# Kernel tuning notes

Measured on AMD Instinct MI355X. Metric: run time of the kernel, lower is better.

Reference implementation:

```python
import jax, jax.numpy as jnp
import numpy as np

Z_DIM = 3
H = 128
N_BLOCKS = 4
N = 30000
E = 180000
T = 2


def _mlp2(x, W1, b1, W2, b2):
    return jnp.maximum(x @ W1 + b1, 0.0) @ W2 + b2


def _stats(x, eps=1e-8):
    # batch mean/std as accumulated by the running-stat Normalizer (buffers -> no grad)
    m = x.mean(0)
    v = jnp.maximum((x * x).mean(0) - m * m, 0.0)
    s = jnp.maximum(jnp.sqrt(v), eps)
    return jax.lax.stop_gradient(m), jax.lax.stop_gradient(s)


def setup_inputs() -> dict:
    key = jax.random.key(0)
    ks = jax.random.split(key, 32)

    def w(k, shape, fan_in):
        return jax.random.normal(k, shape, jnp.float32) / np.sqrt(fan_in).astype(np.float32)

    inp = {}
    inp["z"] = jax.random.normal(ks[0], (T, N, Z_DIM), jnp.float32)
    inp["z_target"] = jax.random.normal(ks[1], (N, Z_DIM), jnp.float32)
    inp["pos"] = jax.random.uniform(ks[2], (N, 2), jnp.float32)
    # encoder node MLP: z_dim -> H -> H
    inp["enc_node_W1"] = w(ks[3], (Z_DIM, H), Z_DIM)
    inp["enc_node_b1"] = jnp.zeros((H,), jnp.float32)
    inp["enc_node_W2"] = w(ks[4], (H, H), H)
    inp["enc_node_b2"] = jnp.zeros((H,), jnp.float32)
    # encoder edge MLP: edge_dim(3) -> H -> H
    inp["enc_edge_W1"] = w(ks[5], (3, H), 3)
    inp["enc_edge_b1"] = jnp.zeros((H,), jnp.float32)
    inp["enc_edge_W2"] = w(ks[6], (H, H), H)
    inp["enc_edge_b2"] = jnp.zeros((H,), jnp.float32)
    # decoder MLP: H -> H -> z_dim
    inp["dec_W1"] = w(ks[7], (H, H), H)
    inp["dec_b1"] = jnp.zeros((H,), jnp.float32)
    inp["dec_W2"] = w(ks[8], (H, Z_DIM), H)
    inp["dec_b2"] = jnp.zeros((Z_DIM,), jnp.float32)
    # GraphNetBlocks, stacked over n_blocks
    inp["blk_edge_W1"] = w(ks[9], (N_BLOCKS, 3 * H, H), 3 * H)
    inp["blk_edge_b1"] = jnp.zeros((N_BLOCKS, H), jnp.float32)
    inp["blk_edge_W2"] = w(ks[10], (N_BLOCKS, H, H), H)
    inp["blk_edge_b2"] = jnp.zeros((N_BLOCKS, H), jnp.float32)
    inp["blk_node_W1"] = w(ks[11], (N_BLOCKS, 2 * H, H), 2 * H)
    inp["blk_node_b1"] = jnp.zeros((N_BLOCKS, H), jnp.float32)
    inp["blk_node_W2"] = w(ks[12], (N_BLOCKS, H, H), H)
    inp["blk_node_b2"] = jnp.zeros((N_BLOCKS, H), jnp.float32)
    # bidirectional mesh edges (triangles_to_edges output)
    inp["senders"] = jax.random.randint(ks[13], (E,), 0, N, jnp.int64)
    inp["receivers"] = jax.random.randint(ks[14], (E,), 0, N, jnp.int64)
    return inp


def reference(z, z_target, pos,
              enc_node_W1, enc_node_b1, enc_node_W2, enc_node_b2,
              enc_edge_W1, enc_edge_b1, enc_edge_W2, enc_edge_b2,
              dec_W1, dec_b1, dec_W2, dec_b2,
              blk_edge_W1, blk_edge_b1, blk_edge_W2, blk_edge_b2,
              blk_node_W1, blk_node_b1, blk_node_W2, blk_node_b2,
              senders, receivers):
    zl = z[-1]                                   # [N, z_dim]
    n_nodes = zl.shape[0]

    # --- build_graph ---
    rel = pos[senders] - pos[receivers]          # [E, 2]
    ef_raw = jnp.concatenate([rel, jnp.linalg.norm(rel, axis=1, keepdims=True)], axis=1)  # [E, 3]
    em, es = _stats(ef_raw)
    ef = _mlp2((ef_raw - em) / es, enc_edge_W1, enc_edge_b1, enc_edge_W2, enc_edge_b2)    # [E, H]
    nm, ns = _stats(zl)
    nf = _mlp2((zl - nm) / ns, enc_node_W1, enc_node_b1, enc_node_W2, enc_node_b2)        # [N, H]

    # --- message passing blocks ---
    def block(carry, p):
        nf, ef = carry
        eW1, eb1, eW2, eb2, nW1, nb1, nW2, nb2 = p
        e_in = jnp.concatenate([ef, nf[senders], nf[receivers]], axis=1)   # [E, 3H]
        ef = _mlp2(e_in, eW1, eb1, eW2, eb2) + ef
        agg = jax.ops.segment_sum(ef, receivers, num_segments=n_nodes)    # [N, H]
        n_in = jnp.concatenate([nf, agg], axis=1)                          # [N, 2H]
        nf = _mlp2(n_in, nW1, nb1, nW2, nb2) + nf
        return (nf, ef), None

    (nf, ef), _ = jax.lax.scan(block, (nf, ef),
                               (blk_edge_W1, blk_edge_b1, blk_edge_W2, blk_edge_b2,
                                blk_node_W1, blk_node_b1, blk_node_W2, blk_node_b2))

    # --- decode + loss ---
    output = _mlp2(nf, dec_W1, dec_b1, dec_W2, dec_b2)                     # [N, z_dim]
    target = z_target - zl
    om, os = _stats(target)
    target_normalized = (target - om) / os
    loss = jnp.mean((target_normalized - output) ** 2)

    z_update = jax.lax.stop_gradient(output) * os + om                     # Normalizer.inverse(detach)
    z_pred = zl + z_update
    rmse = jnp.mean(jnp.sqrt(jnp.mean((z_pred - z_target) ** 2, axis=0)))
    return z_pred, loss, rmse
```

## Files before the change

kernel.cpp:

```cpp
#include <hip/hip_runtime.h>
#include <hip/hip_bf16.h>
#include <math.h>

#define HDIM 128
#define TPB 256

typedef __attribute__((ext_vector_type(8))) short bf16x8;
typedef __attribute__((ext_vector_type(4))) float f32x4;

static inline int ceil_div(int a, int b){ return (a + b - 1) / b; }

__device__ __forceinline__ float wave_sum(float v){
#pragma unroll
  for (int o = 32; o > 0; o >>= 1) v += __shfl_down(v, o, 64);
  return v;
}

__device__ __forceinline__ short f2bf(float f){
  __hip_bfloat16 h = __float2bfloat16(f);
  return *reinterpret_cast<short*>(&h);
}
__device__ __forceinline__ float bfb2f(short s){
  unsigned int u = ((unsigned int)(unsigned short)s) << 16;
  return __builtin_bit_cast(float, u);
}

__device__ __forceinline__ void gl_lds16(const short* g, short* l){
  __builtin_amdgcn_global_load_lds(
      (const __attribute__((address_space(1))) void*)g,
      (__attribute__((address_space(3))) void*)l, 16, 0, 0);
}

__global__ void csr_hist(const int* __restrict__ rcv, int* __restrict__ deg, int E){
  int e = blockIdx.x * blockDim.x + threadIdx.x;
  if (e < E) atomicAdd(&deg[rcv[e]], 1);
}

__global__ void csr_scan(const int* __restrict__ deg, int* __restrict__ row_start,
                         int N, int E){
  __shared__ int part[1024];
  int t = threadIdx.x;
  int chunk = (N + 1023) / 1024;
  int lo = t * chunk, hi = min(lo + chunk, N);
  int s = 0;
  for (int i = lo; i < hi; i++) s += deg[i];
  part[t] = s;
  __syncthreads();
  for (int off = 1; off < 1024; off <<= 1){
    int v = (t >= off) ? part[t - off] : 0;
    __syncthreads();
    part[t] += v;
    __syncthreads();
  }
  int base = (t == 0) ? 0 : part[t - 1];
  for (int i = lo; i < hi; i++){
    row_start[i] = base;
    base += deg[i];
  }
  if (t == 1023) row_start[N] = E;
}

__global__ void edge_prep(const float* __restrict__ pos,
                          const int* __restrict__ snd,
                          const int* __restrict__ rcv,
                          int* __restrict__ cursor,
                          int* __restrict__ psnd,
                          int* __restrict__ prcv,
                          float* __restrict__ ef_raw,
                          float* __restrict__ epart, int E){
  __shared__ float red[4][6];
  int tid = threadIdx.x, w = tid >> 6, l = tid & 63;
  int e = blockIdx.x * blockDim.x + tid;
  float s[6] = {0.f,0.f,0.f,0.f,0.f,0.f};
  if (e < E){
    int si = snd[e], ri = rcv[e];
    int p = atomicAdd(&cursor[ri], 1);
    psnd[p] = si;
    prcv[p] = ri;
    float rx = pos[2*si]   - pos[2*ri];
    float ry = pos[2*si+1] - pos[2*ri+1];
    float nm = sqrtf(rx*rx + ry*ry);
    ef_raw[3*p]   = rx;
    ef_raw[3*p+1] = ry;
    ef_raw[3*p+2] = nm;
    s[0] = rx; s[1] = ry; s[2] = nm;
    s[3] = rx*rx; s[4] = ry*ry; s[5] = nm*nm;
  }
#pragma unroll
  for (int k = 0; k < 6; k++) s[k] = wave_sum(s[k]);
  if (l == 0)
#pragma unroll
    for (int k = 0; k < 6; k++) red[w][k] = s[k];
  __syncthreads();
  if (tid < 6)
    epart[(size_t)blockIdx.x * 6 + tid] =
      red[0][tid] + red[1][tid] + red[2][tid] + red[3][tid];
}

__global__ void node_stats(const float* __restrict__ zl,
                           const float* __restrict__ z_target,
                           float* __restrict__ npart, int N){
  __shared__ float red[4][12];
  int tid = threadIdx.x, w = tid >> 6, l = tid & 63;
  int n = blockIdx.x * blockDim.x + tid;
  float s[12];
#pragma unroll
  for (int i = 0; i < 12; i++) s[i] = 0.f;
  if (n < N){
#pragma unroll
    for (int d = 0; d < 3; d++){
      float z = zl[3*n+d];
      float t = z_target[3*n+d] - z;
      s[d]   = z;  s[3+d] = z*z;
      s[6+d] = t;  s[9+d] = t*t;
    }
  }
#pragma unroll
  for (int i = 0; i < 12; i++) s[i] = wave_sum(s[i]);
  if (l == 0)
#pragma unroll
    for (int i = 0; i < 12; i++) red[w][i] = s[i];
  __syncthreads();
  if (tid < 12)
    npart[(size_t)blockIdx.x * 12 + tid] =
      red[0][tid] + red[1][tid] + red[2][tid] + red[3][tid];
}

__global__ void reduce_stats(const float* __restrict__ ep, int ne,
                             const float* __restrict__ np_, int nn,
                             float* __restrict__ raw){
  __shared__ float red[4];
  int tid = threadIdx.x, w = tid >> 6, l = tid & 63;
  for (int j = 0; j < 6; j++){
    float s = 0.f;
    for (int b = tid; b < ne; b += 256) s += ep[(size_t)b * 6 + j];
    s = wave_sum(s);
    if (l == 0) red[w] = s;
    __syncthreads();
    if (tid == 0) raw[j] = red[0] + red[1] + red[2] + red[3];
    __syncthreads();
  }
  for (int j = 0; j < 12; j++){
    float s = 0.f;
    for (int b = tid; b < nn; b += 256) s += np_[(size_t)b * 12 + j];
    s = wave_sum(s);
    if (l == 0) red[w] = s;
    __syncthreads();
    if (tid == 0) raw[6 + j] = red[0] + red[1] + red[2] + red[3];
    __syncthreads();
  }
}

__global__ void finalize_stats(const float* __restrict__ raw,
                               float* __restrict__ fin, int E, int N){
#pragma unroll
  for (int d = 0; d < 3; d++){
    float cE = (float)E, cN = (float)N;
    float m, v;
    m = raw[0+d] / cE; v = fmaxf(raw[3+d]/cE - m*m, 0.f);
    fin[0+d] = m;  fin[3+d]  = fmaxf(sqrtf(v), 1e-8f);
    m = raw[6+d] / cN; v = fmaxf(raw[9+d]/cN - m*m, 0.f);
    fin[6+d] = m;  fin[9+d]  = fmaxf(sqrtf(v), 1e-8f);
    m = raw[12+d] / cN; v = fmaxf(raw[15+d]/cN - m*m, 0.f);
    fin[12+d] = m; fin[15+d] = fmaxf(sqrtf(v), 1e-8f);
  }
}

__global__ void pack_weights(const float* __restrict__ encEW2,
                             const float* __restrict__ encNW2,
                             const float* __restrict__ decW1,
                             const float* __restrict__ beW1,
                             const float* __restrict__ beW2,
                             const float* __restrict__ bnW1,
                             const float* __restrict__ bnW2,
                             __hip_bfloat16* __restrict__ wp){
  int y = blockIdx.y;
  const float* src; __hip_bfloat16* dst; int K;
  if (y == 0){ src = encEW2; dst = wp;          K = 128; }
  else if (y == 1){ src = encNW2; dst = wp + 16384; K = 128; }
  else if (y == 2){ src = decW1;  dst = wp + 32768; K = 128; }
  else {
    int b = (y - 3) >> 2, j = (y - 3) & 3;
    __hip_bfloat16* base = wp + 49152 + b * 114688;
    if (j == 0){ src = beW1 + b*49152; dst = base;          K = 384; }
    else if (j == 1){ src = beW2 + b*16384; dst = base + 49152; K = 128; }
    else if (j == 2){ src = bnW1 + b*32768; dst = base + 65536; K = 256; }
    else { src = bnW2 + b*16384; dst = base + 98304; K = 128; }
  }
  int id = blockIdx.x * blockDim.x + threadIdx.x;
  if (id >= 128 * K) return;
  int c = id >> 12;
  int r = id & 4095;
  int t = r >> 9;
  int l = (r >> 3) & 63;
  int j = r & 7;
  int k = c * 32 + ((l >> 4) << 3) + j;
  int n = t * 16 + (l & 15);
  dst[id] = __float2bfloat16(src[k * 128 + n]);
}

__launch_bounds__(256)
__global__ void encoder_fused(const float* __restrict__ raw,
                              const float* __restrict__ mptr,
                              const float* __restrict__ sptr,
                              const float* __restrict__ W1,
                              const float* __restrict__ b1,
                              const __hip_bfloat16* __restrict__ W2f,
                              const float* __restrict__ b2,
                              __hip_bfloat16* __restrict__ out, int rows){
  __shared__ __align__(16) short bsh[16384];
  const int tid = threadIdx.x, w = tid >> 6, l = tid & 63, m = l & 15, q = l >> 4;
  const short* wsrc = (const short*)W2f;
#pragma unroll
  for (int i = 0; i < 8; i++){
    int inst = w * 8 + i;
    gl_lds16(wsrc + inst * 512 + l * 8, &bsh[inst * 512]);
  }
  float s0 = mptr[0], s1 = mptr[1], s2 = mptr[2];
  float d0 = sptr[0], d1 = sptr[1], d2 = sptr[2];
  const int row0 = blockIdx.x * 64 + w * 16;
  const int ra = min(row0 + m, rows - 1);
  float x0 = (raw[3*ra]   - s0) / d0;
  float x1 = (raw[3*ra+1] - s1) / d1;
  float x2 = (raw[3*ra+2] - s2) / d2;
  bf16x8 afr[4];
#pragma unroll
  for (int c = 0; c < 4; c++){
    int nb = c * 32 + q * 8;
#pragma unroll
    for (int j = 0; j < 8; j++){
      float h = b1[nb+j] + x0 * W1[nb+j] + x1 * W1[128+nb+j] + x2 * W1[256+nb+j];
      afr[c][j] = f2bf(fmaxf(h, 0.f));
    }
  }
  f32x4 acc[8];
#pragma unroll
  for (int t = 0; t < 8; t++) acc[t] = (f32x4){0.f,0.f,0.f,0.f};
  __syncthreads();
#pragma unroll
  for (int c = 0; c < 4; c++){
#pragma unroll
    for (int t = 0; t < 8; t++){
      bf16x8 b = *(const bf16x8*)&bsh[(c*8 + t)*512 + l*8];
      acc[t] = __builtin_amdgcn_mfma_f32_16x16x32_bf16(afr[c], b, acc[t], 0, 0, 0);
    }
  }
  const int row_d = row0 + q * 4;
#pragma unroll
  for (int t = 0; t < 8; t++){
    int col = t * 16 + m;
    float bb = b2[col];
#pragma unroll
    for (int r = 0; r < 4; r++){
      int e = row_d + r;
      if (e < rows) out[(size_t)e * HDIM + col] = __float2bfloat16(acc[t][r] + bb);
    }
  }
}

__launch_bounds__(256)
__global__ void gemm128_g(const __hip_bfloat16* __restrict__ A,
                          const __hip_bfloat16* __restrict__ Wf,
                          const float* __restrict__ bias,
                          float* __restrict__ out, int rows){
  __shared__ __align__(16) short bsh[16384];
  const int tid = threadIdx.x, w = tid >> 6, l = tid & 63, m = l & 15, q = l >> 4;
  const short* wsrc = (const short*)Wf;
#pragma unroll
  for (int i = 0; i < 8; i++){
    int inst = w * 8 + i;
    gl_lds16(wsrc + inst * 512 + l * 8, &bsh[inst * 512]);
  }
  const int row0 = blockIdx.x * 64 + w * 16;
  const int ra = min(row0 + m, rows - 1);
  const short* pa = (const short*)A + (size_t)ra * HDIM + q * 8;
  bf16x8 afr[4];
#pragma unroll
  for (int c = 0; c < 4; c++) afr[c] = *(const bf16x8*)(pa + c * 32);
  f32x4 acc[8];
#pragma unroll
  for (int t = 0; t < 8; t++) acc[t] = (f32x4){0.f,0.f,0.f,0.f};
  __syncthreads();
#pragma unroll
  for (int c = 0; c < 4; c++){
#pragma unroll
    for (int t = 0; t < 8; t++){
      bf16x8 b = *(const bf16x8*)&bsh[(c*8 + t)*512 + l*8];
      acc[t] = __builtin_amdgcn_mfma_f32_16x16x32_bf16(afr[c], b, acc[t], 0, 0, 0);
    }
  }
  const int row_d = row0 + q * 4;
#pragma unroll
  for (int t = 0; t < 8; t++){
    int col = t * 16 + m;
    float bb = bias[col];
#pragma unroll
    for (int r = 0; r < 4; r++){
      int e = row_d + r;
      if (e < rows) out[(size_t)e * HDIM + col] = fmaxf(acc[t][r] + bb, 0.f);
    }
  }
}

__launch_bounds__(512)
__global__ void edge_block(const int* __restrict__ psnd,
                           const int* __restrict__ prcv,
                           const __hip_bfloat16* __restrict__ nf,
                           __hip_bfloat16* __restrict__ ef,
                           const __hip_bfloat16* __restrict__ Wfrag,
                           const float* __restrict__ b1,
                           const float* __restrict__ b2,
                           int E){
  __shared__ __align__(16) short bsh[2][4096];
  __shared__ __align__(16) short hsh[8][16][136];
  const int tid = threadIdx.x, w = tid >> 6, l = tid & 63, m = l & 15, q = l >> 4;
  const short* wsrc = (const short*)Wfrag;
  gl_lds16(wsrc + w*512 + l*8, &bsh[0][w*512]);

  const int row0 = blockIdx.x * 128 + w * 16;
  const int ra = min(row0 + m, E - 1);
  const int si = psnd[ra], ri = prcv[ra];
  const short* pe = (const short*)ef + (size_t)ra * HDIM + q * 8;
  const short* ps = (const short*)nf + (size_t)si * HDIM + q * 8;
  const short* pr = (const short*)nf + (size_t)ri * HDIM + q * 8;
  bf16x8 afr[12];
#pragma unroll
  for (int c = 0; c < 4; c++){
    afr[c]   = *(const bf16x8*)(pe + c * 32);
    afr[4+c] = *(const bf16x8*)(ps + c * 32);
    afr[8+c] = *(const bf16x8*)(pr + c * 32);
  }
  const int orow = row0 + (l >> 2);
  const int orc = min(orow, E - 1);
  const short* pold = (const short*)ef + (size_t)orc * HDIM + (l & 3) * 32;
  bf16x8 vold[4];
#pragma unroll
  for (int k = 0; k < 4; k++) vold[k] = *(const bf16x8*)(pold + k * 8);

  f32x4 acc[8];
#pragma unroll
  for (int t = 0; t < 8; t++) acc[t] = (f32x4){0.f,0.f,0.f,0.f};
  __syncthreads();
#pragma unroll
  for (int c = 0; c < 12; c++){
    if (c + 1 < 12)
      gl_lds16(wsrc + (c+1)*4096 + w*512 + l*8, &bsh[(c+1)&1][w*512]);
    const short* bb = &bsh[c & 1][0];
#pragma unroll
    for (int t = 0; t < 8; t++){
      bf16x8 b = *(const bf16x8*)(bb + t*512 + l*8);
      acc[t] = __builtin_amdgcn_mfma_f32_16x16x32_bf16(afr[c], b, acc[t], 0, 0, 0);
    }
    if (c + 1 < 12) __syncthreads();
  }
#pragma unroll
  for (int t = 0; t < 8; t++){
    float bb = b1[t * 16 + m];
#pragma unroll
    for (int r = 0; r < 4; r++)
      hsh[w][q*4 + r][t*16 + m] = f2bf(fmaxf(acc[t][r] + bb, 0.f));
  }
  const short* ph = &hsh[w][m][0] + q * 8;
  const short* w2 = wsrc + 49152;
  f32x4 acc2[8];
#pragma unroll
  for (int t = 0; t < 8; t++) acc2[t] = (f32x4){0.f,0.f,0.f,0.f};
#pragma unroll
  for (int c = 0; c < 4; c++){
    bf16x8 a = *(const bf16x8*)(ph + c * 32);
#pragma unroll
    for (int t = 0; t < 8; t++){
      bf16x8 b = *(const bf16x8*)(w2 + ((c*8 + t)*64 + l)*8);
      acc2[t] = __builtin_amdgcn_mfma_f32_16x16x32_bf16(a, b, acc2[t], 0, 0, 0);
    }
  }
#pragma unroll
  for (int t = 0; t < 8; t++){
    float bb = b2[t * 16 + m];
#pragma unroll
    for (int r = 0; r < 4; r++)
      hsh[w][q*4 + r][t*16 + m] = f2bf(acc2[t][r] + bb);
  }
  if (orow < E){
    const short* src = &hsh[w][l >> 2][(l & 3) * 32];
    short* dst = (short*)ef + (size_t)orow * HDIM + (l & 3) * 32;
#pragma unroll
    for (int k = 0; k < 4; k++){
      bf16x8 vnew = *(const bf16x8*)(src + k * 8);
      bf16x8 vo;
#pragma unroll
      for (int j = 0; j < 8; j++) vo[j] = f2bf(bfb2f(vnew[j]) + bfb2f(vold[k][j]));
      *(bf16x8*)(dst + k * 8) = vo;
    }
  }
}

__launch_bounds__(512)
__global__ void node_block(const int* __restrict__ row_start,
                           const __hip_bfloat16* __restrict__ ef,
                           __hip_bfloat16* __restrict__ nf,
                           const __hip_bfloat16* __restrict__ Wfrag,
                           const float* __restrict__ b1,
                           const float* __restrict__ b2,
                           int N){
  __shared__ __align__(16) short bsh[2][4096];
  __shared__ __align__(16) short hsh[8][16][136];
  const int tid = threadIdx.x, w = tid >> 6, l = tid & 63, m = l & 15, q = l >> 4;
  const short* wsrc = (const short*)Wfrag;
  gl_lds16(wsrc + w*512 + l*8, &bsh[0][w*512]);

  const int row0 = blockIdx.x * 128 + w * 16;
  const int ra = min(row0 + m, N - 1);
  const short* pn = (const short*)nf + (size_t)ra * HDIM + q * 8;
  bf16x8 afr[8];
#pragma unroll
  for (int c = 0; c < 4; c++) afr[c] = *(const bf16x8*)(pn + c * 32);
  const int orow = row0 + (l >> 2);
  const int orc = min(orow, N - 1);
  const short* pold = (const short*)nf + (size_t)orc * HDIM + (l & 3) * 32;
  bf16x8 vold[4];
#pragma unroll
  for (int k = 0; k < 4; k++) vold[k] = *(const bf16x8*)(pold + k * 8);

  float sum[4][8];
#pragma unroll
  for (int c = 0; c < 4; c++)
#pragma unroll
    for (int j = 0; j < 8; j++) sum[c][j] = 0.f;
  int s0 = row_start[ra], s1 = row_start[ra + 1];
  for (int it = s0; it < s1; it++){
    const short* pf = (const short*)ef + (size_t)it * HDIM + q * 8;
#pragma unroll
    for (int c = 0; c < 4; c++){
      bf16x8 v = *(const bf16x8*)(pf + c * 32);
#pragma unroll
      for (int j = 0; j < 8; j++) sum[c][j] += bfb2f(v[j]);
    }
  }
#pragma unroll
  for (int c = 0; c < 4; c++)
#pragma unroll
    for (int j = 0; j < 8; j++) afr[4 + c][j] = f2bf(sum[c][j]);

  f32x4 acc[8];
#pragma unroll
  for (int t = 0; t < 8; t++) acc[t] = (f32x4){0.f,0.f,0.f,0.f};
  __syncthreads();
#pragma unroll
  for (int c = 0; c < 8; c++){
    if (c + 1 < 8)
      gl_lds16(wsrc + (c+1)*4096 + w*512 + l*8, &bsh[(c+1)&1][w*512]);
    const short* bb = &bsh[c & 1][0];
#pragma unroll
    for (int t = 0; t < 8; t++){
      bf16x8 b = *(const bf16x8*)(bb + t*512 + l*8);
      acc[t] = __builtin_amdgcn_mfma_f32_16x16x32_bf16(afr[c], b, acc[t], 0, 0, 0);
    }
    if (c + 1 < 8) __syncthreads();
  }
#pragma unroll
  for (int t = 0; t < 8; t++){
    float bb = b1[t * 16 + m];
#pragma unroll
    for (int r = 0; r < 4; r++)
      hsh[w][q*4 + r][t*16 + m] = f2bf(fmaxf(acc[t][r] + bb, 0.f));
  }
  const short* ph = &hsh[w][m][0] + q * 8;
  const short* w2 = wsrc + 32768;
  f32x4 acc2[8];
#pragma unroll
  for (int t = 0; t < 8; t++) acc2[t] = (f32x4){0.f,0.f,0.f,0.f};
#pragma unroll
  for (int c = 0; c < 4; c++){
    bf16x8 a = *(const bf16x8*)(ph + c * 32);
#pragma unroll
    for (int t = 0; t < 8; t++){
      bf16x8 b = *(const bf16x8*)(w2 + ((c*8 + t)*64 + l)*8);
      acc2[t] = __builtin_amdgcn_mfma_f32_16x16x32_bf16(a, b, acc2[t], 0, 0, 0);
    }
  }
#pragma unroll
  for (int t = 0; t < 8; t++){
    float bb = b2[t * 16 + m];
#pragma unroll
    for (int r = 0; r < 4; r++)
      hsh[w][q*4 + r][t*16 + m] = f2bf(acc2[t][r] + bb);
  }
  if (orow < N){
    const short* src = &hsh[w][l >> 2][(l & 3) * 32];
    short* dst = (short*)nf + (size_t)orow * HDIM + (l & 3) * 32;
#pragma unroll
    for (int k = 0; k < 4; k++){
      bf16x8 vnew = *(const bf16x8*)(src + k * 8);
      bf16x8 vo;
#pragma unroll
      for (int j = 0; j < 8; j++) vo[j] = f2bf(bfb2f(vnew[j]) + bfb2f(vold[k][j]));
      *(bf16x8*)(dst + k * 8) = vo;
    }
  }
}

__global__ void dec_final(const float* __restrict__ hbuf,
                          const float* __restrict__ W2,
                          const float* __restrict__ b2,
                          float* __restrict__ outd, int rows){
  __shared__ float hl[64 * 129];
  __shared__ float Wl[HDIM * 3];
  __shared__ float bl[3];
  int t = threadIdx.x;
  int node0 = blockIdx.x * 64;
  for (int i = t; i < HDIM * 3; i += 256) Wl[i] = W2[i];
  if (t < 3) bl[t] = b2[t];
#pragma unroll
  for (int i = 0; i < 32; i++){
    int lin = t + i * 256;
    int r = lin >> 7;
    int c = lin & 127;
    int node = node0 + r;
    hl[r * 129 + c] = (node < rows) ? hbuf[(size_t)node * HDIM + c] : 0.f;
  }
  __syncthreads();
  if (t < 64){
    int node = node0 + t;
    if (node < rows){
      float a0 = bl[0], a1 = bl[1], a2 = bl[2];
      for (int k = 0; k < HDIM; k++){
        float v = hl[t * 129 + k];
        a0 += v * Wl[k * 3];
        a1 += v * Wl[k * 3 + 1];
        a2 += v * Wl[k * 3 + 2];
      }
      outd[3 * node]     = a0;
      outd[3 * node + 1] = a1;
      outd[3 * node + 2] = a2;
    }
  }
}

__global__ void epilogue(const float* __restrict__ dec_out,
                         const float* __restrict__ zl,
                         const float* __restrict__ z_target,
                         const float* __restrict__ fin,
                         float* __restrict__ d_out,
                         float* __restrict__ lpart, int N){
  __shared__ float red[4][4];
  int tid = threadIdx.x, w = tid >> 6, l = tid & 63;
  int n = blockIdx.x * blockDim.x + tid;
  float s[4] = {0.f,0.f,0.f,0.f};
  if (n < N){
#pragma unroll
    for (int d = 0; d < 3; d++){
      float om = fin[12 + d], os = fin[15 + d];
      float o   = dec_out[3*n + d];
      float zld = zl[3*n + d];
      float zt  = z_target[3*n + d];
      float tgt = zt - zld;
      float tn  = (tgt - om) / os;
      float diff = tn - o;
      s[0] += diff * diff;
      float zp = zld + o * os + om;
      d_out[3*n + d] = zp;
      float e = zp - zt;
      s[1 + d] = e * e;
    }
  }
#pragma unroll
  for (int k = 0; k < 4; k++) s[k] = wave_sum(s[k]);
  if (l == 0)
#pragma unroll
    for (int k = 0; k < 4; k++) red[w][k] = s[k];
  __syncthreads();
  if (tid < 4)
    lpart[(size_t)blockIdx.x * 4 + tid] =
      red[0][tid] + red[1][tid] + red[2][tid] + red[3][tid];
}

__global__ void finalize_out(const float* __restrict__ lpart, int nb,
                             float* __restrict__ d_out, int N){
  __shared__ float red[4];
  __shared__ float vals[4];
  int tid = threadIdx.x, w = tid >> 6, l = tid & 63;
  for (int j = 0; j < 4; j++){
    float s = 0.f;
    for (int b = tid; b < nb; b += 256) s += lpart[(size_t)b * 4 + j];
    s = wave_sum(s);
    if (l == 0) red[w] = s;
    __syncthreads();
    if (tid == 0) vals[j] = red[0] + red[1] + red[2] + red[3];
    __syncthreads();
  }
  if (tid == 0){
    float cN = (float)N;
    float loss = vals[0] / (3.f * cN);
    float rmse = (sqrtf(vals[1] / cN) + sqrtf(vals[2] / cN) + sqrtf(vals[3] / cN)) / 3.f;
    d_out[(size_t)3 * N]     = loss;
    d_out[(size_t)3 * N + 1] = rmse;
  }
}

extern "C" void kernel_launch(void* const* d_in, const int* in_sizes, int n_in,
                              void* d_out, int out_size, void* d_ws, size_t ws_size,
                              hipStream_t stream){
  const float* z           = (const float*)d_in[0];
  const float* z_target    = (const float*)d_in[1];
  const float* pos         = (const float*)d_in[2];
  const float* enc_node_W1 = (const float*)d_in[3];
  const float* enc_node_b1 = (const float*)d_in[4];
  const float* enc_node_W2 = (const float*)d_in[5];
  const float* enc_node_b2 = (const float*)d_in[6];
  const float* enc_edge_W1 = (const float*)d_in[7];
  const float* enc_edge_b1 = (const float*)d_in[8];
  const float* enc_edge_W2 = (const float*)d_in[9];
  const float* enc_edge_b2 = (const float*)d_in[10];
  const float* dec_W1      = (const float*)d_in[11];
  const float* dec_b1      = (const float*)d_in[12];
  const float* dec_W2      = (const float*)d_in[13];
  const float* dec_b2      = (const float*)d_in[14];
  const float* blk_edge_W1 = (const float*)d_in[15];
  const float* blk_edge_b1 = (const float*)d_in[16];
  const float* blk_edge_W2 = (const float*)d_in[17];
  const float* blk_edge_b2 = (const float*)d_in[18];
  const float* blk_node_W1 = (const float*)d_in[19];
  const float* blk_node_b1 = (const float*)d_in[20];
  const float* blk_node_W2 = (const float*)d_in[21];
  const float* blk_node_b2 = (const float*)d_in[22];
  const int*   senders     = (const int*)d_in[23];
  const int*   receivers   = (const int*)d_in[24];

  const int N = in_sizes[1] / 3;
  const int E = in_sizes[23];
  const float* zl = z + (size_t)N * 3;

  const int neb = ceil_div(E, TPB);
  const int nnb = ceil_div(N, TPB);

  char* p = (char*)d_ws;
  auto carve = [&](size_t bytes) -> char* {
    char* r = p; p += (bytes + 255) & ~(size_t)255; return r;
  };
  float* stats_raw = (float*)carve(32 * 4);
  float* stats_fin = (float*)carve(32 * 4);
  float* epart     = (float*)carve((size_t)neb * 6 * 4);
  float* npart     = (float*)carve((size_t)nnb * 12 * 4);
  float* lpart     = (float*)carve((size_t)nnb * 4 * 4);
  float* ef_raw    = (float*)carve((size_t)E * 3 * 4);
  float* dec_out   = (float*)carve((size_t)N * 3 * 4);
  float* hbuf      = (float*)carve((size_t)N * HDIM * 4);
  int*   deg       = (int*)carve((size_t)N * 4);
  int*   row_start = (int*)carve((size_t)(N + 1) * 4);
  int*   cursor    = (int*)carve((size_t)N * 4);
  int*   psnd      = (int*)carve((size_t)E * 4);
  int*   prcv      = (int*)carve((size_t)E * 4);
  __hip_bfloat16* wp = (__hip_bfloat16*)carve((size_t)507904 * 2);
  __hip_bfloat16* ef = (__hip_bfloat16*)carve((size_t)E * HDIM * 2);
  __hip_bfloat16* nf = (__hip_bfloat16*)carve((size_t)N * HDIM * 2);

  float* out = (float*)d_out;

  hipMemsetAsync(deg, 0, (size_t)N * 4, stream);

  csr_hist<<<neb, TPB, 0, stream>>>(receivers, deg, E);
  csr_scan<<<1, 1024, 0, stream>>>(deg, row_start, N, E);
  hipMemcpyAsync(cursor, row_start, (size_t)N * 4, hipMemcpyDeviceToDevice, stream);
  edge_prep<<<neb, TPB, 0, stream>>>(pos, senders, receivers, cursor,
                                     psnd, prcv, ef_raw, epart, E);

  node_stats<<<nnb, TPB, 0, stream>>>(zl, z_target, npart, N);
  reduce_stats<<<1, TPB, 0, stream>>>(epart, neb, npart, nnb, stats_raw);
  finalize_stats<<<1, 1, 0, stream>>>(stats_raw, stats_fin, E, N);

  pack_weights<<<dim3(192, 19), TPB, 0, stream>>>(enc_edge_W2, enc_node_W2, dec_W1,
                                                  blk_edge_W1, blk_edge_W2,
                                                  blk_node_W1, blk_node_W2, wp);

  encoder_fused<<<ceil_div(E, 64), TPB, 0, stream>>>(ef_raw, stats_fin + 0, stats_fin + 3,
                                                     enc_edge_W1, enc_edge_b1,
                                                     wp, enc_edge_b2, ef, E);
  encoder_fused<<<ceil_div(N, 64), TPB, 0, stream>>>(zl, stats_fin + 6, stats_fin + 9,
                                                     enc_node_W1, enc_node_b1,
                                                     wp + 16384, enc_node_b2, nf, N);

  for (int b = 0; b < 4; b++){
    const __hip_bfloat16* eWf = wp + 49152 + (size_t)b * 114688;
    const __hip_bfloat16* nWf = eWf + 65536;
    const float* eb1 = blk_edge_b1 + (size_t)b * 128;
    const float* eb2 = blk_edge_b2 + (size_t)b * 128;
    const float* nb1 = blk_node_b1 + (size_t)b * 128;
    const float* nb2 = blk_node_b2 + (size_t)b * 128;

    edge_block<<<ceil_div(E, 128), 512, 0, stream>>>(psnd, prcv, nf, ef,
                                                     eWf, eb1, eb2, E);
    node_block<<<ceil_div(N, 128), 512, 0, stream>>>(row_start, ef, nf,
                                                     nWf, nb1, nb2, N);
  }

  gemm128_g<<<ceil_div(N, 64), TPB, 0, stream>>>(nf, wp + 32768, dec_b1, hbuf, N);
  dec_final<<<ceil_div(N, 64), TPB, 0, stream>>>(hbuf, dec_W2, dec_b2, dec_out, N);

  epilogue<<<nnb, TPB, 0, stream>>>(dec_out, zl, z_target, stats_fin,
                                    out, lpart, N);
  finalize_out<<<1, TPB, 0, stream>>>(lpart, nnb, out, N);
}
```

Measured before the change: 561.3 us.

## Precompute per-node sender/receiver projections before the edge MLP

The first edge-MLP layer is split by linearity: the sender and receiver slices of W1 are applied once per node in a new msg_pre kernel, producing a [N,256] buffer. The edge kernel gathers and adds the two projected rows in place of the raw node features, and its per-edge GEMM shrinks from K=384 to K=128. This cuts edge-level MFMA work by about two thirds. In exchange it adds a kernel launch per block and an extra bf16 rounding of the projected sums, which changes numerics slightly.

```diff
diff --git a/kernel.cpp b/kernel.cpp
--- a/kernel.cpp
+++ b/kernel.cpp
@@ -303,9 +303,52 @@
 }
 
 __launch_bounds__(512)
+__global__ void msg_pre(const __hip_bfloat16* __restrict__ nf,
+                        const __hip_bfloat16* __restrict__ eWf,
+                        __hip_bfloat16* __restrict__ u, int N){
+  __shared__ __align__(16) short wsh[32768];
+  const int tid = threadIdx.x, w = tid >> 6, l = tid & 63, m = l & 15, q = l >> 4;
+  const short* wsrc = (const short*)eWf + 4 * 4096;
+#pragma unroll
+  for (int i = 0; i < 8; i++){
+    int inst = w * 8 + i;
+    gl_lds16(wsrc + inst * 512 + l * 8, &wsh[inst * 512]);
+  }
+  const int row0 = blockIdx.x * 128 + w * 16;
+  const int ra = min(row0 + m, N - 1);
+  const short* pa = (const short*)nf + (size_t)ra * HDIM + q * 8;
+  bf16x8 afr[4];
+#pragma unroll
+  for (int c = 0; c < 4; c++) afr[c] = *(const bf16x8*)(pa + c * 32);
+  f32x4 acc[16];
+#pragma unroll
+  for (int t = 0; t < 16; t++) acc[t] = (f32x4){0.f,0.f,0.f,0.f};
+  __syncthreads();
+#pragma unroll
+  for (int c = 0; c < 4; c++){
+#pragma unroll
+    for (int t = 0; t < 16; t++){
+      int cc = (t < 8) ? c : (4 + c);
+      bf16x8 b = *(const bf16x8*)&wsh[cc * 4096 + (t & 7) * 512 + l * 8];
+      acc[t] = __builtin_amdgcn_mfma_f32_16x16x32_bf16(afr[c], b, acc[t], 0, 0, 0);
+    }
+  }
+  const int row_d = row0 + q * 4;
+#pragma unroll
+  for (int t = 0; t < 16; t++){
+    int col = t * 16 + m;
+#pragma unroll
+    for (int r = 0; r < 4; r++){
+      int n = row_d + r;
+      if (n < N) u[(size_t)n * 256 + col] = __float2bfloat16(acc[t][r]);
+    }
+  }
+}
+
+__launch_bounds__(512)
 __global__ void edge_block(const int* __restrict__ psnd,
                            const int* __restrict__ prcv,
-                           const __hip_bfloat16* __restrict__ nf,
+                           const __hip_bfloat16* __restrict__ u,
                            __hip_bfloat16* __restrict__ ef,
                            const __hip_bfloat16* __restrict__ Wfrag,
                            const float* __restrict__ b1,
@@ -319,16 +362,26 @@
 
   const int row0 = blockIdx.x * 128 + w * 16;
   const int ra = min(row0 + m, E - 1);
-  const int si = psnd[ra], ri = prcv[ra];
   const short* pe = (const short*)ef + (size_t)ra * HDIM + q * 8;
-  const short* ps = (const short*)nf + (size_t)si * HDIM + q * 8;
-  const short* pr = (const short*)nf + (size_t)ri * HDIM + q * 8;
-  bf16x8 afr[12];
-#pragma unroll
-  for (int c = 0; c < 4; c++){
-    afr[c]   = *(const bf16x8*)(pe + c * 32);
-    afr[4+c] = *(const bf16x8*)(ps + c * 32);
-    afr[8+c] = *(const bf16x8*)(pr + c * 32);
+  bf16x8 afr[4];
+#pragma unroll
+  for (int c = 0; c < 4; c++) afr[c] = *(const bf16x8*)(pe + c * 32);
+
+  {
+    int grow = min(row0 + (l >> 2), E - 1);
+    int us_row = psnd[grow], ur_row = prcv[grow];
+    const short* pus = (const short*)u + (size_t)us_row * 256 + (l & 3) * 32;
+    const short* pur = (const short*)u + (size_t)ur_row * 256 + 128 + (l & 3) * 32;
+    short* hdst = &hsh[w][l >> 2][(l & 3) * 32];
+#pragma unroll
+    for (int k = 0; k < 4; k++){
+      bf16x8 a = *(const bf16x8*)(pus + k * 8);
+      bf16x8 b = *(const bf16x8*)(pur + k * 8);
+      bf16x8 s;
+#pragma unroll
+      for (int j = 0; j < 8; j++) s[j] = f2bf(bfb2f(a[j]) + bfb2f(b[j]));
+      *(bf16x8*)(hdst + k * 8) = s;
+    }
   }
   const int orow = row0 + (l >> 2);
   const int orc = min(orow, E - 1);
@@ -342,8 +395,8 @@
   for (int t = 0; t < 8; t++) acc[t] = (f32x4){0.f,0.f,0.f,0.f};
   __syncthreads();
 #pragma unroll
-  for (int c = 0; c < 12; c++){
-    if (c + 1 < 12)
+  for (int c = 0; c < 4; c++){
+    if (c + 1 < 4)
       gl_lds16(wsrc + (c+1)*4096 + w*512 + l*8, &bsh[(c+1)&1][w*512]);
     const short* bb = &bsh[c & 1][0];
 #pragma unroll
@@ -351,14 +404,16 @@
       bf16x8 b = *(const bf16x8*)(bb + t*512 + l*8);
       acc[t] = __builtin_amdgcn_mfma_f32_16x16x32_bf16(afr[c], b, acc[t], 0, 0, 0);
     }
-    if (c + 1 < 12) __syncthreads();
+    if (c + 1 < 4) __syncthreads();
   }
 #pragma unroll
   for (int t = 0; t < 8; t++){
     float bb = b1[t * 16 + m];
 #pragma unroll
-    for (int r = 0; r < 4; r++)
-      hsh[w][q*4 + r][t*16 + m] = f2bf(fmaxf(acc[t][r] + bb, 0.f));
+    for (int r = 0; r < 4; r++){
+      float uval = bfb2f(hsh[w][q*4 + r][t*16 + m]);
+      hsh[w][q*4 + r][t*16 + m] = f2bf(fmaxf(acc[t][r] + uval + bb, 0.f));
+    }
   }
   const short* ph = &hsh[w][m][0] + q * 8;
   const short* w2 = wsrc + 49152;
@@ -654,6 +709,7 @@
   __hip_bfloat16* wp = (__hip_bfloat16*)carve((size_t)507904 * 2);
   __hip_bfloat16* ef = (__hip_bfloat16*)carve((size_t)E * HDIM * 2);
   __hip_bfloat16* nf = (__hip_bfloat16*)carve((size_t)N * HDIM * 2);
+  __hip_bfloat16* u  = (__hip_bfloat16*)carve((size_t)N * 256 * 2);
 
   float* out = (float*)d_out;
 
@@ -688,7 +744,8 @@
     const float* nb1 = blk_node_b1 + (size_t)b * 128;
     const float* nb2 = blk_node_b2 + (size_t)b * 128;
 
-    edge_block<<<ceil_div(E, 128), 512, 0, stream>>>(psnd, prcv, nf, ef,
+    msg_pre<<<ceil_div(N, 128), 512, 0, stream>>>(nf, eWf, u, N);
+    edge_block<<<ceil_div(E, 128), 512, 0, stream>>>(psnd, prcv, u, ef,
                                                      eWf, eb1, eb2, E);
     node_block<<<ceil_div(N, 128), 512, 0, stream>>>(row_start, ef, nf,
                                                      nWf, nb1, nb2, N);
```

After: 556.9 us. Within noise of the previous version (-0.8%).
